# Kernel optimization log

Hardware: AMD Instinct MI355X
Metric: run time of the kernel (lower is better)

The kernel has to match this reference:

```python
import jax, jax.numpy as jnp
import numpy as np

EPS = 1e-5

def conv3x3(x, W, b):
    # NCHW 3x3 conv, padding=1 (SAME)
    y = jax.lax.conv_general_dilated(x, W, (1, 1), ((1, 1), (1, 1)),
                                     dimension_numbers=('NCHW', 'OIHW', 'NCHW'))
    return y + b[None, :, None, None]

def bn_relu(x, gamma, beta):
    # BatchNorm2d in training mode: batch statistics over (N,H,W)
    m = x.mean(axis=(0, 2, 3), keepdims=True)
    v = x.var(axis=(0, 2, 3), keepdims=True)
    xn = (x - m) * jax.lax.rsqrt(v + EPS)
    return jax.nn.relu(xn * gamma[None, :, None, None] + beta[None, :, None, None])

def haar_dwt2(x):
    # pywt.dwt2(x, 'db1') for even H,W: cA=LL, cH=row-detail/col-approx,
    # cV=row-approx/col-detail, cD=HH; each 0.5*(+-a +-b +-c +-d)
    a = x[:, :, 0::2, 0::2]
    b = x[:, :, 0::2, 1::2]
    c = x[:, :, 1::2, 0::2]
    d = x[:, :, 1::2, 1::2]
    cA = (a + b + c + d) * 0.5
    cH = (a + b - c - d) * 0.5
    cV = (a - b + c - d) * 0.5
    cD = (a - b - c + d) * 0.5
    return jnp.concatenate([cA, cH, cV, cD], axis=1)  # [B, 4C, H/2, W/2]

def setup_inputs() -> dict:
    key = jax.random.key(0)
    ks = jax.random.split(key, 4)
    B, Cin, Cout, H, W = 8, 64, 128, 256, 256
    inputs = jax.random.normal(ks[0], (B, Cin, H, W), dtype=jnp.float32)
    W1 = jax.random.normal(ks[1], (Cout, Cin, 3, 3), dtype=jnp.float32) * 0.05
    W2 = jax.random.normal(ks[2], (Cout, Cout, 3, 3), dtype=jnp.float32) * 0.05
    W3 = jax.random.normal(ks[3], (Cout, 4 * Cout, 3, 3), dtype=jnp.float32) * 0.05
    z = jnp.zeros((Cout,), jnp.float32)
    o = jnp.ones((Cout,), jnp.float32)
    return {"inputs": inputs,
            "W1": W1, "b1": z, "g1": o, "be1": z,
            "W2": W2, "b2": z, "g2": o, "be2": z,
            "W3": W3, "b3": z, "g3": o, "be3": z}

def reference(inputs, W1, b1, g1, be1, W2, b2, g2, be2, W3, b3, g3, be3):
    h = bn_relu(conv3x3(inputs, W1, b1), g1, be1)
    skip_con = bn_relu(conv3x3(h, W2, b2), g2, be2)          # [B, out_c, H, W]
    # original detaches before the pywt round-trip
    dwt = haar_dwt2(jax.lax.stop_gradient(skip_con))          # [B, 4*out_c, H/2, W/2]
    dwt_out = bn_relu(conv3x3(dwt, W3, b3), g3, be3)          # [B, out_c, H/2, W/2]
    return (skip_con, dwt_out)
```

## Files before the change

### kernel.cpp

```cpp
#include <hip/hip_runtime.h>

typedef __attribute__((ext_vector_type(8))) short bf16x8;
typedef __attribute__((ext_vector_type(4))) short bf16x4;
typedef __attribute__((ext_vector_type(4))) float f32x4;

__device__ __forceinline__ float bf2f(ushort u) {
  union { unsigned int i; float f; } v; v.i = ((unsigned int)u) << 16; return v.f;
}
__device__ __forceinline__ ushort f2bf(float f) {
  union { float f; unsigned int i; } v; v.f = f;
  unsigned int x = v.i;
  unsigned int r = (x + 0x7fffu + ((x >> 16) & 1u)) >> 16;
  return (ushort)r;
}

__global__ void zero_f32(float* p, int n) {
  int i = blockIdx.x * 256 + threadIdx.x;
  if (i < n) p[i] = 0.f;
}

__global__ void pack_w(const float* __restrict__ W, ushort* __restrict__ Wp, int Cin) {
  int ncic = Cin >> 5;
  int total = 9 * ncic * 8 * 64 * 8;
  for (int idx = blockIdx.x * 256 + threadIdx.x; idx < total; idx += gridDim.x * 256) {
    int j = idx & 7;
    int l = (idx >> 3) & 63;
    int cf = (idx >> 9) & 7;
    int rest = idx >> 12;
    int cic = rest % ncic;
    int tap = rest / ncic;
    int co = cf * 16 + (l & 15);
    int ci = cic * 32 + ((l >> 4) * 8) + j;
    int ky = tap / 3, kx = tap % 3;
    Wp[idx] = f2bf(W[((co * Cin + ci) * 3 + ky) * 3 + kx]);
  }
}

__global__ __launch_bounds__(256)
void nchw2nhwc(const float* __restrict__ in, ushort* __restrict__ out) {
  const int n  = blockIdx.y;
  const int p0 = blockIdx.x << 6;
  const int tid = threadIdx.x;
  __shared__ ushort t[64 * 72];
  {
    int c  = tid >> 2;
    int pq = (tid & 3) << 4;
    const float* ip = in + (((size_t)(n * 64 + c)) << 16) + p0 + pq;
#pragma unroll
    for (int k = 0; k < 4; ++k) {
      float4 f = *(const float4*)(ip + k * 4);
      int p = pq + k * 4;
      t[(p + 0) * 72 + c] = f2bf(f.x);
      t[(p + 1) * 72 + c] = f2bf(f.y);
      t[(p + 2) * 72 + c] = f2bf(f.z);
      t[(p + 3) * 72 + c] = f2bf(f.w);
    }
  }
  __syncthreads();
#pragma unroll
  for (int k = 0; k < 2; ++k) {
    int id = k * 256 + tid;
    int cj = id & 7, p = id >> 3;
    bf16x8 v = *(const bf16x8*)&t[p * 72 + cj * 8];
    *(bf16x8*)(out + ((((size_t)n << 16) + p0 + p) << 6) + cj * 8) = v;
  }
}

__device__ __forceinline__ bf16x8 bnrelu8(bf16x8 v, const float* __restrict__ coef, int c0) {
  float4 a0 = *(const float4*)(coef + c0);
  float4 a1 = *(const float4*)(coef + c0 + 4);
  float4 b0 = *(const float4*)(coef + 128 + c0);
  float4 b1 = *(const float4*)(coef + 128 + c0 + 4);
  bf16x8 r;
  r[0] = (short)f2bf(fmaxf(a0.x * bf2f((ushort)v[0]) + b0.x, 0.f));
  r[1] = (short)f2bf(fmaxf(a0.y * bf2f((ushort)v[1]) + b0.y, 0.f));
  r[2] = (short)f2bf(fmaxf(a0.z * bf2f((ushort)v[2]) + b0.z, 0.f));
  r[3] = (short)f2bf(fmaxf(a0.w * bf2f((ushort)v[3]) + b0.w, 0.f));
  r[4] = (short)f2bf(fmaxf(a1.x * bf2f((ushort)v[4]) + b1.x, 0.f));
  r[5] = (short)f2bf(fmaxf(a1.y * bf2f((ushort)v[5]) + b1.y, 0.f));
  r[6] = (short)f2bf(fmaxf(a1.z * bf2f((ushort)v[6]) + b1.z, 0.f));
  r[7] = (short)f2bf(fmaxf(a1.w * bf2f((ushort)v[7]) + b1.w, 0.f));
  return r;
}

template<int MODE>
__global__ __launch_bounds__(256)
void conv_mfma(const ushort* __restrict__ src, const ushort* __restrict__ Wp,
               const float* __restrict__ bias, const float* __restrict__ coef,
               ushort* __restrict__ out, float* __restrict__ sSum, float* __restrict__ sSsq,
               int Cin, int H, int W)
{
  const int ncic = Cin >> 5;
  const int x0 = blockIdx.x << 6;
  const int y0 = blockIdx.y << 1;
  const int n  = blockIdx.z;
  const int tid = threadIdx.x;
  const int wv = tid >> 6, l = tid & 63, l15 = l & 15, l4 = l >> 4;

  __shared__ __align__(16) char smem[17408];
  ushort* lds = (ushort*)smem;
  ushort* eps = (ushort*)smem;

  f32x4 acc[2][2][4];
#pragma unroll
  for (int yr = 0; yr < 2; ++yr)
#pragma unroll
    for (int f = 0; f < 2; ++f)
#pragma unroll
      for (int xf = 0; xf < 4; ++xf) acc[yr][f][xf] = (f32x4){0.f, 0.f, 0.f, 0.f};

  const size_t HW = (size_t)H * W;

  for (int cic = 0; cic < ncic; ++cic) {
    __syncthreads();
    for (int i = tid; i < 1056; i += 256) {
      int cj = i & 3;
      int t = i >> 2;
      int row = t / 66;
      int xt = t - row * 66;
      int ry = y0 + row - 1;
      int gx = x0 + xt - 1;
      bf16x8 v = {};
      if ((unsigned)ry < (unsigned)H && (unsigned)gx < (unsigned)W) {
        const ushort* p = src + ((size_t)n * HW + (size_t)ry * W + gx) * Cin + (cic << 5) + (cj << 3);
        v = *(const bf16x8*)p;
        if (MODE == 1) v = bnrelu8(v, coef, (cic << 5) + (cj << 3));
      }
      *(bf16x8*)&lds[(((row << 2) | cj) * 66 + xt) << 3] = v;
    }
    __syncthreads();

#pragma unroll
    for (int tap = 0; tap < 9; ++tap) {
      const int ky = tap / 3, kx = tap % 3;
      bf16x8 afr[2];
#pragma unroll
      for (int f = 0; f < 2; ++f) {
        const int cf = (wv << 1) | f;
        afr[f] = *(const bf16x8*)(Wp + (((size_t)(tap * ncic + cic) * 8 + cf) * 64 + l) * 8);
      }
      bf16x8 bfr[2][4];
#pragma unroll
      for (int yr = 0; yr < 2; ++yr)
#pragma unroll
        for (int xf = 0; xf < 4; ++xf) {
          int row = yr + ky;
          int xt = (xf << 4) + l15 + kx;
          bfr[yr][xf] = *(const bf16x8*)&lds[(((row << 2) | l4) * 66 + xt) << 3];
        }
#pragma unroll
      for (int f = 0; f < 2; ++f)
#pragma unroll
        for (int yr = 0; yr < 2; ++yr)
#pragma unroll
          for (int xf = 0; xf < 4; ++xf)
            acc[yr][f][xf] = __builtin_amdgcn_mfma_f32_16x16x32_bf16(afr[f], bfr[yr][xf], acc[yr][f][xf], 0, 0, 0);
    }
  }

  float sm[2][4] = {{0.f}}, sq[2][4] = {{0.f}};
  const int cb = (wv << 5) + (l4 << 2);
  for (int yr = 0; yr < 2; ++yr) {
    __syncthreads();
#pragma unroll
    for (int f = 0; f < 2; ++f) {
      const int cf = cb + (f << 4);
      float4 bv = *(const float4*)(bias + cf);
#pragma unroll
      for (int xf = 0; xf < 4; ++xf) {
        float v0 = acc[yr][f][xf][0] + bv.x;
        float v1 = acc[yr][f][xf][1] + bv.y;
        float v2 = acc[yr][f][xf][2] + bv.z;
        float v3 = acc[yr][f][xf][3] + bv.w;
        sm[f][0] += v0; sq[f][0] += v0 * v0;
        sm[f][1] += v1; sq[f][1] += v1 * v1;
        sm[f][2] += v2; sq[f][2] += v2 * v2;
        sm[f][3] += v3; sq[f][3] += v3 * v3;
        bf16x4 u;
        u[0] = (short)f2bf(v0); u[1] = (short)f2bf(v1);
        u[2] = (short)f2bf(v2); u[3] = (short)f2bf(v3);
        *(bf16x4*)&eps[((xf << 4) + l15) * 136 + cf] = u;
      }
    }
    __syncthreads();
    {
      const int xx = tid >> 2, c0 = (tid & 3) << 5;
      ushort* op = out + ((size_t)n * HW + (size_t)(y0 + yr) * W + x0 + xx) * 128 + c0;
#pragma unroll
      for (int k = 0; k < 4; ++k) {
        bf16x8 v = *(const bf16x8*)&eps[xx * 136 + c0 + (k << 3)];
        *(bf16x8*)(op + (k << 3)) = v;
      }
    }
  }

  const int rep = (int)((blockIdx.z * gridDim.y + blockIdx.y) * gridDim.x + blockIdx.x) & 31;
#pragma unroll
  for (int f = 0; f < 2; ++f)
#pragma unroll
    for (int j = 0; j < 4; ++j) {
      float s = sm[f][j], q = sq[f][j];
#pragma unroll
      for (int o = 1; o < 16; o <<= 1) { s += __shfl_xor(s, o); q += __shfl_xor(q, o); }
      if (l15 == 0) {
        int co = cb + (f << 4) + j;
        atomicAdd(&sSum[rep * 128 + co], s);
        atomicAdd(&sSsq[rep * 128 + co], q);
      }
    }
}

__global__ void bn_finalize(const float* __restrict__ sSum, const float* __restrict__ sSsq,
                            const float* __restrict__ g, const float* __restrict__ be,
                            float* __restrict__ coef, float invN)
{
  int c = threadIdx.x;
  float S = 0.f, Q = 0.f;
  for (int r = 0; r < 32; ++r) { S += sSum[r * 128 + c]; Q += sSsq[r * 128 + c]; }
  float m = S * invN;
  float v = Q * invN - m * m;
  float a = g[c] / sqrtf(v + 1e-5f);
  coef[c] = a;
  coef[128 + c] = be[c] - m * a;
}

__global__ __launch_bounds__(256)
void bn_transpose_out(const ushort* __restrict__ src, const float* __restrict__ coef,
                      float* __restrict__ dst, int H, int W)
{
  const int n  = blockIdx.z >> 2;
  const int cc = blockIdx.z & 3;
  const int x0 = blockIdx.x << 6;
  const int y  = blockIdx.y;
  const int tid = threadIdx.x;
  __shared__ float t[32 * 68];
  const size_t HW = (size_t)H * W;
  {
    int p = tid >> 2, cj = tid & 3;
    int c0 = (cc << 5) + (cj << 3);
    bf16x8 v = *(const bf16x8*)(src + ((size_t)n * HW + (size_t)y * W + x0 + p) * 128 + c0);
    float4 a0 = *(const float4*)(coef + c0);
    float4 a1 = *(const float4*)(coef + c0 + 4);
    float4 b0 = *(const float4*)(coef + 128 + c0);
    float4 b1 = *(const float4*)(coef + 128 + c0 + 4);
    int cl = cj << 3;
    t[(cl + 0) * 68 + p] = fmaxf(a0.x * bf2f((ushort)v[0]) + b0.x, 0.f);
    t[(cl + 1) * 68 + p] = fmaxf(a0.y * bf2f((ushort)v[1]) + b0.y, 0.f);
    t[(cl + 2) * 68 + p] = fmaxf(a0.z * bf2f((ushort)v[2]) + b0.z, 0.f);
    t[(cl + 3) * 68 + p] = fmaxf(a0.w * bf2f((ushort)v[3]) + b0.w, 0.f);
    t[(cl + 4) * 68 + p] = fmaxf(a1.x * bf2f((ushort)v[4]) + b1.x, 0.f);
    t[(cl + 5) * 68 + p] = fmaxf(a1.y * bf2f((ushort)v[5]) + b1.y, 0.f);
    t[(cl + 6) * 68 + p] = fmaxf(a1.z * bf2f((ushort)v[6]) + b1.z, 0.f);
    t[(cl + 7) * 68 + p] = fmaxf(a1.w * bf2f((ushort)v[7]) + b1.w, 0.f);
  }
  __syncthreads();
  {
    int c = tid >> 3, x8 = (tid & 7) << 3;
    float4 r0 = *(const float4*)&t[c * 68 + x8];
    float4 r1 = *(const float4*)&t[c * 68 + x8 + 4];
    float* op = dst + ((size_t)(n * 128 + (cc << 5) + c)) * HW + (size_t)y * W + x0 + x8;
    *(float4*)op = r0;
    *(float4*)(op + 4) = r1;
  }
}

__global__ __launch_bounds__(256)
void dwt_nhwc(const ushort* __restrict__ src, const float* __restrict__ coef,
              ushort* __restrict__ dwt)
{
  int idx = blockIdx.x * 256 + threadIdx.x;
  int cj = idx & 15;
  int ox = (idx >> 4) & 127;
  int oy = (idx >> 11) & 127;
  int n  = idx >> 18;
  int c0 = cj << 3;
  size_t base = (((size_t)n << 16) + (size_t)(oy * 2) * 256 + ox * 2) * 128 + c0;
  bf16x8 u00 = *(const bf16x8*)(src + base);
  bf16x8 u01 = *(const bf16x8*)(src + base + 128);
  bf16x8 u10 = *(const bf16x8*)(src + base + 256 * 128);
  bf16x8 u11 = *(const bf16x8*)(src + base + 256 * 128 + 128);
  float4 a0 = *(const float4*)(coef + c0);
  float4 a1 = *(const float4*)(coef + c0 + 4);
  float4 b0 = *(const float4*)(coef + 128 + c0);
  float4 b1 = *(const float4*)(coef + 128 + c0 + 4);
  float av[8] = {a0.x, a0.y, a0.z, a0.w, a1.x, a1.y, a1.z, a1.w};
  float bv[8] = {b0.x, b0.y, b0.z, b0.w, b1.x, b1.y, b1.z, b1.w};
  bf16x8 oA, oH, oV, oD;
#pragma unroll
  for (int k = 0; k < 8; ++k) {
    float p00 = fmaxf(av[k] * bf2f((ushort)u00[k]) + bv[k], 0.f);
    float p01 = fmaxf(av[k] * bf2f((ushort)u01[k]) + bv[k], 0.f);
    float p10 = fmaxf(av[k] * bf2f((ushort)u10[k]) + bv[k], 0.f);
    float p11 = fmaxf(av[k] * bf2f((ushort)u11[k]) + bv[k], 0.f);
    oA[k] = (short)f2bf((p00 + p01 + p10 + p11) * 0.5f);
    oH[k] = (short)f2bf((p00 + p01 - p10 - p11) * 0.5f);
    oV[k] = (short)f2bf((p00 - p01 + p10 - p11) * 0.5f);
    oD[k] = (short)f2bf((p00 - p01 - p10 + p11) * 0.5f);
  }
  size_t db = (((size_t)n << 14) + oy * 128 + ox) * 512 + c0;
  *(bf16x8*)(dwt + db)       = oA;
  *(bf16x8*)(dwt + db + 128) = oH;
  *(bf16x8*)(dwt + db + 256) = oV;
  *(bf16x8*)(dwt + db + 384) = oD;
}

extern "C" void kernel_launch(void* const* d_in, const int* in_sizes, int n_in,
                              void* d_out, int out_size, void* d_ws, size_t ws_size,
                              hipStream_t stream)
{
  const float* input = (const float*)d_in[0];
  const float* W1  = (const float*)d_in[1];
  const float* b1  = (const float*)d_in[2];
  const float* g1  = (const float*)d_in[3];
  const float* be1 = (const float*)d_in[4];
  const float* W2  = (const float*)d_in[5];
  const float* b2  = (const float*)d_in[6];
  const float* g2  = (const float*)d_in[7];
  const float* be2 = (const float*)d_in[8];
  const float* W3  = (const float*)d_in[9];
  const float* b3  = (const float*)d_in[10];
  const float* g3  = (const float*)d_in[11];
  const float* be3 = (const float*)d_in[12];

  char* ws = (char*)d_ws;
  ushort* h_raw    = (ushort*)(ws + 0);
  ushort* skip_raw = (ushort*)(ws + 134217728);
  ushort* dwt      = (ushort*)(ws + 268435456);
  ushort* in_nhwc  = (ushort*)(ws + 268435456);
  ushort* raw3     = (ushort*)(ws + 402653184);
  float*  stats    = (float*)(ws + 436207616);
  float*  s1 = stats,          *q1 = stats + 4096;
  float*  s2 = stats + 8192,   *q2 = stats + 12288;
  float*  s3 = stats + 16384,  *q3 = stats + 20480;
  float*  coef = (float*)(ws + 436305920);
  float*  c1 = coef, *c2 = coef + 256, *c3 = coef + 512;
  ushort* Wp1 = (ushort*)(ws + 436308992);
  ushort* Wp2 = (ushort*)(ws + 436456448);
  ushort* Wp3 = (ushort*)(ws + 436751360);

  zero_f32<<<96, 256, 0, stream>>>(stats, 24576);
  pack_w<<<288, 256, 0, stream>>>(W1, Wp1, 64);
  pack_w<<<576, 256, 0, stream>>>(W2, Wp2, 128);
  pack_w<<<2304, 256, 0, stream>>>(W3, Wp3, 512);
  nchw2nhwc<<<dim3(1024, 8), 256, 0, stream>>>(input, in_nhwc);

  conv_mfma<0><<<dim3(4, 128, 8), 256, 0, stream>>>(in_nhwc, Wp1, b1, nullptr,
                                                    h_raw, s1, q1, 64, 256, 256);
  bn_finalize<<<1, 128, 0, stream>>>(s1, q1, g1, be1, c1, 1.f / 524288.f);

  conv_mfma<1><<<dim3(4, 128, 8), 256, 0, stream>>>(h_raw, Wp2, b2, c1,
                                                    skip_raw, s2, q2, 128, 256, 256);
  bn_finalize<<<1, 128, 0, stream>>>(s2, q2, g2, be2, c2, 1.f / 524288.f);

  bn_transpose_out<<<dim3(4, 256, 32), 256, 0, stream>>>(skip_raw, c2, (float*)d_out, 256, 256);
  dwt_nhwc<<<8192, 256, 0, stream>>>(skip_raw, c2, dwt);

  conv_mfma<0><<<dim3(2, 64, 8), 256, 0, stream>>>(dwt, Wp3, b3, nullptr,
                                                   raw3, s3, q3, 512, 128, 128);
  bn_finalize<<<1, 128, 0, stream>>>(s3, q3, g3, be3, c3, 1.f / 131072.f);

  bn_transpose_out<<<dim3(2, 128, 32), 256, 0, stream>>>(raw3, c3, (float*)d_out + 67108864, 128, 128);
}
```

Before: 726.6 us.

## Double-buffer conv LDS tiles, prefetch fragments, and fuse skip output with DWT

The conv kernel now double-buffers its input tile in shared memory. The next channel chunk is loaded into registers while the current one is computed, which drops one barrier per chunk. Work is remapped so each wave owns one output row and four 16-channel fragments, and weight and LDS fragments for the next tap are prefetched. Separately, the skip BN/ReLU transpose output and the Haar DWT are fused into one kernel so skip_raw is read once instead of twice. The cost is more registers and twice the LDS per block, which may reduce occupancy.

```diff
diff --git a/kernel.cpp b/kernel.cpp
--- a/kernel.cpp
+++ b/kernel.cpp
@@ -96,90 +96,127 @@
   const int n  = blockIdx.z;
   const int tid = threadIdx.x;
   const int wv = tid >> 6, l = tid & 63, l15 = l & 15, l4 = l >> 4;
-
-  __shared__ __align__(16) char smem[17408];
-  ushort* lds = (ushort*)smem;
-  ushort* eps = (ushort*)smem;
-
-  f32x4 acc[2][2][4];
-#pragma unroll
-  for (int yr = 0; yr < 2; ++yr)
-#pragma unroll
-    for (int f = 0; f < 2; ++f)
-#pragma unroll
-      for (int xf = 0; xf < 4; ++xf) acc[yr][f][xf] = (f32x4){0.f, 0.f, 0.f, 0.f};
+  const int cg = wv >> 1;
+  const int wy = wv & 1;
+  const int cg4 = cg << 2;
+
+  __shared__ __align__(16) ushort smem[2 * 8448];
 
   const size_t HW = (size_t)H * W;
-
+  const ushort* srcn = src + (size_t)n * HW * Cin;
+
+  f32x4 acc[4][4];
+#pragma unroll
+  for (int f = 0; f < 4; ++f)
+#pragma unroll
+    for (int xf = 0; xf < 4; ++xf) acc[f][xf] = (f32x4){0.f, 0.f, 0.f, 0.f};
+
+  bf16x8 st[5];
+
+  auto LOADREG = [&](int cic) {
+#pragma unroll
+    for (int it = 0; it < 5; ++it) {
+      if (it < 4 || tid < 32) {
+        int i = it * 256 + tid;
+        int cj = i & 3, p = i >> 2;
+        int row = p / 66, xt = p - row * 66;
+        int ry = y0 + row - 1, gx = x0 + xt - 1;
+        bf16x8 v = {};
+        if ((unsigned)ry < (unsigned)H && (unsigned)gx < (unsigned)W)
+          v = *(const bf16x8*)(srcn + ((size_t)ry * W + gx) * Cin + (cic << 5) + (cj << 3));
+        st[it] = v;
+      }
+    }
+  };
+
+  auto WRITE = [&](ushort* buf, int cic) {
+#pragma unroll
+    for (int it = 0; it < 5; ++it) {
+      if (it < 4 || tid < 32) {
+        int i = it * 256 + tid;
+        bf16x8 v = st[it];
+        if (MODE == 1) {
+          int cj = i & 3, p = i >> 2;
+          int row = p / 66, xt = p - row * 66;
+          int ry = y0 + row - 1, gx = x0 + xt - 1;
+          if ((unsigned)ry < (unsigned)H && (unsigned)gx < (unsigned)W)
+            v = bnrelu8(v, coef, (cic << 5) + (cj << 3));
+        }
+        *(bf16x8*)(buf + i * 8) = v;
+      }
+    }
+  };
+
+  auto COMPUTE = [&](const ushort* buf, int cic) {
+    const ushort* lrow = buf + l15 * 32 + l4 * 8;
+    const ushort* wp = Wp + ((size_t)cic * 8 + cg4) * 512 + (size_t)l * 8;
+    const size_t tapstride = (size_t)ncic * 8 * 512;
+    bf16x8 aC[4], bC[4], aN[4], bN[4];
+#pragma unroll
+    for (int f = 0; f < 4; ++f) aC[f] = *(const bf16x8*)(wp + f * 512);
+#pragma unroll
+    for (int xf = 0; xf < 4; ++xf)
+      bC[xf] = *(const bf16x8*)(lrow + (wy * 66 + xf * 16) * 32);
+#pragma unroll
+    for (int tap = 0; tap < 9; ++tap) {
+      if (tap < 8) {
+        const int ky1 = (tap + 1) / 3, kx1 = (tap + 1) % 3;
+#pragma unroll
+        for (int f = 0; f < 4; ++f)
+          aN[f] = *(const bf16x8*)(wp + (size_t)(tap + 1) * tapstride + f * 512);
+#pragma unroll
+        for (int xf = 0; xf < 4; ++xf)
+          bN[xf] = *(const bf16x8*)(lrow + ((wy + ky1) * 66 + xf * 16 + kx1) * 32);
+      }
+#pragma unroll
+      for (int f = 0; f < 4; ++f)
+#pragma unroll
+        for (int xf = 0; xf < 4; ++xf)
+          acc[f][xf] = __builtin_amdgcn_mfma_f32_16x16x32_bf16(aC[f], bC[xf], acc[f][xf], 0, 0, 0);
+#pragma unroll
+      for (int f = 0; f < 4; ++f) aC[f] = aN[f];
+#pragma unroll
+      for (int xf = 0; xf < 4; ++xf) bC[xf] = bN[xf];
+    }
+  };
+
+  LOADREG(0);
+  WRITE(smem, 0);
+  __syncthreads();
+
+  int cur = 0;
   for (int cic = 0; cic < ncic; ++cic) {
+    if (cic + 1 < ncic) LOADREG(cic + 1);
+    COMPUTE(smem + cur * 8448, cic);
+    if (cic + 1 < ncic) WRITE(smem + (cur ^ 1) * 8448, cic + 1);
     __syncthreads();
-    for (int i = tid; i < 1056; i += 256) {
-      int cj = i & 3;
-      int t = i >> 2;
-      int row = t / 66;
-      int xt = t - row * 66;
-      int ry = y0 + row - 1;
-      int gx = x0 + xt - 1;
-      bf16x8 v = {};
-      if ((unsigned)ry < (unsigned)H && (unsigned)gx < (unsigned)W) {
-        const ushort* p = src + ((size_t)n * HW + (size_t)ry * W + gx) * Cin + (cic << 5) + (cj << 3);
-        v = *(const bf16x8*)p;
-        if (MODE == 1) v = bnrelu8(v, coef, (cic << 5) + (cj << 3));
-      }
-      *(bf16x8*)&lds[(((row << 2) | cj) * 66 + xt) << 3] = v;
-    }
-    __syncthreads();
-
-#pragma unroll
-    for (int tap = 0; tap < 9; ++tap) {
-      const int ky = tap / 3, kx = tap % 3;
-      bf16x8 afr[2];
-#pragma unroll
-      for (int f = 0; f < 2; ++f) {
-        const int cf = (wv << 1) | f;
-        afr[f] = *(const bf16x8*)(Wp + (((size_t)(tap * ncic + cic) * 8 + cf) * 64 + l) * 8);
-      }
-      bf16x8 bfr[2][4];
-#pragma unroll
-      for (int yr = 0; yr < 2; ++yr)
-#pragma unroll
-        for (int xf = 0; xf < 4; ++xf) {
-          int row = yr + ky;
-          int xt = (xf << 4) + l15 + kx;
-          bfr[yr][xf] = *(const bf16x8*)&lds[(((row << 2) | l4) * 66 + xt) << 3];
-        }
-#pragma unroll
-      for (int f = 0; f < 2; ++f)
-#pragma unroll
-        for (int yr = 0; yr < 2; ++yr)
-#pragma unroll
-          for (int xf = 0; xf < 4; ++xf)
-            acc[yr][f][xf] = __builtin_amdgcn_mfma_f32_16x16x32_bf16(afr[f], bfr[yr][xf], acc[yr][f][xf], 0, 0, 0);
-    }
-  }
-
-  float sm[2][4] = {{0.f}}, sq[2][4] = {{0.f}};
-  const int cb = (wv << 5) + (l4 << 2);
+    cur ^= 1;
+  }
+
+  float smv[4][4] = {{0.f}}, sqv[4][4] = {{0.f}};
+  ushort* eps = smem;
   for (int yr = 0; yr < 2; ++yr) {
     __syncthreads();
-#pragma unroll
-    for (int f = 0; f < 2; ++f) {
-      const int cf = cb + (f << 4);
-      float4 bv = *(const float4*)(bias + cf);
-#pragma unroll
-      for (int xf = 0; xf < 4; ++xf) {
-        float v0 = acc[yr][f][xf][0] + bv.x;
-        float v1 = acc[yr][f][xf][1] + bv.y;
-        float v2 = acc[yr][f][xf][2] + bv.z;
-        float v3 = acc[yr][f][xf][3] + bv.w;
-        sm[f][0] += v0; sq[f][0] += v0 * v0;
-        sm[f][1] += v1; sq[f][1] += v1 * v1;
-        sm[f][2] += v2; sq[f][2] += v2 * v2;
-        sm[f][3] += v3; sq[f][3] += v3 * v3;
-        bf16x4 u;
-        u[0] = (short)f2bf(v0); u[1] = (short)f2bf(v1);
-        u[2] = (short)f2bf(v2); u[3] = (short)f2bf(v3);
-        *(bf16x4*)&eps[((xf << 4) + l15) * 136 + cf] = u;
+    if (wy == yr) {
+#pragma unroll
+      for (int f = 0; f < 4; ++f) {
+        const int col = (cg << 6) + (f << 4) + (l4 << 2);
+        float4 bv = *(const float4*)(bias + col);
+#pragma unroll
+        for (int xf = 0; xf < 4; ++xf) {
+          float v0 = acc[f][xf][0] + bv.x;
+          float v1 = acc[f][xf][1] + bv.y;
+          float v2 = acc[f][xf][2] + bv.z;
+          float v3 = acc[f][xf][3] + bv.w;
+          smv[f][0] += v0; sqv[f][0] += v0 * v0;
+          smv[f][1] += v1; sqv[f][1] += v1 * v1;
+          smv[f][2] += v2; sqv[f][2] += v2 * v2;
+          smv[f][3] += v3; sqv[f][3] += v3 * v3;
+          bf16x4 u;
+          u[0] = (short)f2bf(v0); u[1] = (short)f2bf(v1);
+          u[2] = (short)f2bf(v2); u[3] = (short)f2bf(v3);
+          *(bf16x4*)&eps[((xf << 4) + l15) * 136 + col] = u;
+        }
       }
     }
     __syncthreads();
@@ -187,23 +224,21 @@
       const int xx = tid >> 2, c0 = (tid & 3) << 5;
       ushort* op = out + ((size_t)n * HW + (size_t)(y0 + yr) * W + x0 + xx) * 128 + c0;
 #pragma unroll
-      for (int k = 0; k < 4; ++k) {
-        bf16x8 v = *(const bf16x8*)&eps[xx * 136 + c0 + (k << 3)];
-        *(bf16x8*)(op + (k << 3)) = v;
-      }
+      for (int k = 0; k < 4; ++k)
+        *(bf16x8*)(op + (k << 3)) = *(const bf16x8*)&eps[xx * 136 + c0 + (k << 3)];
     }
   }
 
   const int rep = (int)((blockIdx.z * gridDim.y + blockIdx.y) * gridDim.x + blockIdx.x) & 31;
 #pragma unroll
-  for (int f = 0; f < 2; ++f)
+  for (int f = 0; f < 4; ++f)
 #pragma unroll
     for (int j = 0; j < 4; ++j) {
-      float s = sm[f][j], q = sq[f][j];
+      float s = smv[f][j], q = sqv[f][j];
 #pragma unroll
       for (int o = 1; o < 16; o <<= 1) { s += __shfl_xor(s, o); q += __shfl_xor(q, o); }
       if (l15 == 0) {
-        int co = cb + (f << 4) + j;
+        int co = (cg << 6) + (f << 4) + (l4 << 2) + j;
         atomicAdd(&sSum[rep * 128 + co], s);
         atomicAdd(&sSsq[rep * 128 + co], q);
       }
@@ -222,6 +257,73 @@
   float a = g[c] / sqrtf(v + 1e-5f);
   coef[c] = a;
   coef[128 + c] = be[c] - m * a;
+}
+
+__global__ __launch_bounds__(256)
+void skip_dwt2(const ushort* __restrict__ skipRaw, const float* __restrict__ coef,
+               float* __restrict__ outSkip, ushort* __restrict__ dwt)
+{
+  const int x0 = blockIdx.x << 6;
+  const int oy = blockIdx.y;
+  const int n  = blockIdx.z >> 2;
+  const int ct = blockIdx.z & 3;
+  const int y0 = oy << 1;
+  const int tid = threadIdx.x;
+  __shared__ float t32[32 * 2 * 68];
+
+#pragma unroll
+  for (int it = 0; it < 2; ++it) {
+    int i = it * 256 + tid;
+    int cj = i & 3, x = (i >> 2) & 63, r = i >> 8;
+    int c0 = (ct << 5) + (cj << 3);
+    bf16x8 v = *(const bf16x8*)(skipRaw + (((size_t)n << 16) + (size_t)(y0 + r) * 256 + x0 + x) * 128 + c0);
+    float4 a0 = *(const float4*)(coef + c0);
+    float4 a1 = *(const float4*)(coef + c0 + 4);
+    float4 b0 = *(const float4*)(coef + 128 + c0);
+    float4 b1 = *(const float4*)(coef + 128 + c0 + 4);
+    float av[8] = {a0.x, a0.y, a0.z, a0.w, a1.x, a1.y, a1.z, a1.w};
+    float bv[8] = {b0.x, b0.y, b0.z, b0.w, b1.x, b1.y, b1.z, b1.w};
+    int cl = cj << 3;
+#pragma unroll
+    for (int k = 0; k < 8; ++k)
+      t32[((cl + k) * 2 + r) * 68 + x] = fmaxf(av[k] * bf2f((ushort)v[k]) + bv[k], 0.f);
+  }
+  __syncthreads();
+
+  {
+    int c = tid >> 3, x8 = (tid & 7) << 3;
+    float* op = outSkip + (((size_t)(n * 128 + (ct << 5) + c)) << 16) + (size_t)y0 * 256 + x0 + x8;
+#pragma unroll
+    for (int r = 0; r < 2; ++r) {
+      float4 r0 = *(const float4*)&t32[(c * 2 + r) * 68 + x8];
+      float4 r1 = *(const float4*)&t32[(c * 2 + r) * 68 + x8 + 4];
+      *(float4*)(op + (size_t)r * 256) = r0;
+      *(float4*)(op + (size_t)r * 256 + 4) = r1;
+    }
+  }
+
+  if (tid < 128) {
+    int cj = tid & 3, ox = tid >> 2;
+    int cl = cj << 3;
+    bf16x8 oA, oH, oV, oD;
+#pragma unroll
+    for (int k = 0; k < 8; ++k) {
+      int c = cl + k;
+      float p00 = t32[(c * 2 + 0) * 68 + 2 * ox];
+      float p01 = t32[(c * 2 + 0) * 68 + 2 * ox + 1];
+      float p10 = t32[(c * 2 + 1) * 68 + 2 * ox];
+      float p11 = t32[(c * 2 + 1) * 68 + 2 * ox + 1];
+      oA[k] = (short)f2bf((p00 + p01 + p10 + p11) * 0.5f);
+      oH[k] = (short)f2bf((p00 + p01 - p10 - p11) * 0.5f);
+      oV[k] = (short)f2bf((p00 - p01 + p10 - p11) * 0.5f);
+      oD[k] = (short)f2bf((p00 - p01 - p10 + p11) * 0.5f);
+    }
+    size_t db = ((size_t)n * 16384 + (size_t)oy * 128 + (x0 >> 1) + ox) * 512 + (ct << 5) + cl;
+    *(bf16x8*)(dwt + db)       = oA;
+    *(bf16x8*)(dwt + db + 128) = oH;
+    *(bf16x8*)(dwt + db + 256) = oV;
+    *(bf16x8*)(dwt + db + 384) = oD;
+  }
 }
 
 __global__ __launch_bounds__(256)
@@ -264,46 +366,6 @@
   }
 }
 
-__global__ __launch_bounds__(256)
-void dwt_nhwc(const ushort* __restrict__ src, const float* __restrict__ coef,
-              ushort* __restrict__ dwt)
-{
-  int idx = blockIdx.x * 256 + threadIdx.x;
-  int cj = idx & 15;
-  int ox = (idx >> 4) & 127;
-  int oy = (idx >> 11) & 127;
-  int n  = idx >> 18;
-  int c0 = cj << 3;
-  size_t base = (((size_t)n << 16) + (size_t)(oy * 2) * 256 + ox * 2) * 128 + c0;
-  bf16x8 u00 = *(const bf16x8*)(src + base);
-  bf16x8 u01 = *(const bf16x8*)(src + base + 128);
-  bf16x8 u10 = *(const bf16x8*)(src + base + 256 * 128);
-  bf16x8 u11 = *(const bf16x8*)(src + base + 256 * 128 + 128);
-  float4 a0 = *(const float4*)(coef + c0);
-  float4 a1 = *(const float4*)(coef + c0 + 4);
-  float4 b0 = *(const float4*)(coef + 128 + c0);
-  float4 b1 = *(const float4*)(coef + 128 + c0 + 4);
-  float av[8] = {a0.x, a0.y, a0.z, a0.w, a1.x, a1.y, a1.z, a1.w};
-  float bv[8] = {b0.x, b0.y, b0.z, b0.w, b1.x, b1.y, b1.z, b1.w};
-  bf16x8 oA, oH, oV, oD;
-#pragma unroll
-  for (int k = 0; k < 8; ++k) {
-    float p00 = fmaxf(av[k] * bf2f((ushort)u00[k]) + bv[k], 0.f);
-    float p01 = fmaxf(av[k] * bf2f((ushort)u01[k]) + bv[k], 0.f);
-    float p10 = fmaxf(av[k] * bf2f((ushort)u10[k]) + bv[k], 0.f);
-    float p11 = fmaxf(av[k] * bf2f((ushort)u11[k]) + bv[k], 0.f);
-    oA[k] = (short)f2bf((p00 + p01 + p10 + p11) * 0.5f);
-    oH[k] = (short)f2bf((p00 + p01 - p10 - p11) * 0.5f);
-    oV[k] = (short)f2bf((p00 - p01 + p10 - p11) * 0.5f);
-    oD[k] = (short)f2bf((p00 - p01 - p10 + p11) * 0.5f);
-  }
-  size_t db = (((size_t)n << 14) + oy * 128 + ox) * 512 + c0;
-  *(bf16x8*)(dwt + db)       = oA;
-  *(bf16x8*)(dwt + db + 128) = oH;
-  *(bf16x8*)(dwt + db + 256) = oV;
-  *(bf16x8*)(dwt + db + 384) = oD;
-}
-
 extern "C" void kernel_launch(void* const* d_in, const int* in_sizes, int n_in,
                               void* d_out, int out_size, void* d_ws, size_t ws_size,
                               hipStream_t stream)
@@ -352,8 +414,7 @@
                                                     skip_raw, s2, q2, 128, 256, 256);
   bn_finalize<<<1, 128, 0, stream>>>(s2, q2, g2, be2, c2, 1.f / 524288.f);
 
-  bn_transpose_out<<<dim3(4, 256, 32), 256, 0, stream>>>(skip_raw, c2, (float*)d_out, 256, 256);
-  dwt_nhwc<<<8192, 256, 0, stream>>>(skip_raw, c2, dwt);
+  skip_dwt2<<<dim3(4, 128, 32), 256, 0, stream>>>(skip_raw, c2, (float*)d_out, dwt);
 
   conv_mfma<0><<<dim3(2, 64, 8), 256, 0, stream>>>(dwt, Wp3, b3, nullptr,
                                                    raw3, s3, q3, 512, 128, 128);
```

After: 992.9 us. 1.37x slower.

## Fuse skip BN-transpose output with Haar DWT and repack weights per-lane

Applied to the files above, without the earlier changes.

Merges the skip-connection BN+ReLU NCHW write and the Haar DWT into one kernel that reads each two-row tile of the raw conv output once, normalizes it into LDS, and emits both the fp32 skip output and the bf16 DWT coefficients. This removes a second full read of skip_raw and one kernel launch. Separately, the packed weight layout is reordered so each lane's nine taps and two fragments sit contiguously, giving a simpler base pointer and more local weight loads in the conv inner loop. The fused kernel uses more shared memory per block and only half the threads do the DWT stage.

```diff
diff --git a/kernel.cpp b/kernel.cpp
--- a/kernel.cpp
+++ b/kernel.cpp
@@ -21,16 +21,18 @@
 
 __global__ void pack_w(const float* __restrict__ W, ushort* __restrict__ Wp, int Cin) {
   int ncic = Cin >> 5;
-  int total = 9 * ncic * 8 * 64 * 8;
+  int total = ncic * 4 * 64 * 9 * 2 * 8;
   for (int idx = blockIdx.x * 256 + threadIdx.x; idx < total; idx += gridDim.x * 256) {
     int j = idx & 7;
-    int l = (idx >> 3) & 63;
-    int cf = (idx >> 9) & 7;
-    int rest = idx >> 12;
-    int cic = rest % ncic;
-    int tap = rest / ncic;
-    int co = cf * 16 + (l & 15);
-    int ci = cic * 32 + ((l >> 4) * 8) + j;
+    int f = (idx >> 3) & 1;
+    int rest = idx >> 4;
+    int tap = rest % 9;  rest /= 9;
+    int l = rest & 63;
+    int pc = rest >> 6;
+    int pair = pc & 3;
+    int cic = pc >> 2;
+    int co = ((pair << 1) | f) * 16 + (l & 15);
+    int ci = (cic << 5) + ((l >> 4) << 3) + j;
     int ky = tap / 3, kx = tap % 3;
     Wp[idx] = f2bf(W[((co * Cin + ci) * 3 + ky) * 3 + kx]);
   }
@@ -130,15 +132,15 @@
     }
     __syncthreads();
 
+    const ushort* wp = Wp + (((size_t)(cic * 4 + wv) * 64 + l) * 144);
+
 #pragma unroll
     for (int tap = 0; tap < 9; ++tap) {
       const int ky = tap / 3, kx = tap % 3;
       bf16x8 afr[2];
 #pragma unroll
-      for (int f = 0; f < 2; ++f) {
-        const int cf = (wv << 1) | f;
-        afr[f] = *(const bf16x8*)(Wp + (((size_t)(tap * ncic + cic) * 8 + cf) * 64 + l) * 8);
-      }
+      for (int f = 0; f < 2; ++f)
+        afr[f] = *(const bf16x8*)(wp + (tap * 2 + f) * 8);
       bf16x8 bfr[2][4];
 #pragma unroll
       for (int yr = 0; yr < 2; ++yr)
@@ -187,10 +189,8 @@
       const int xx = tid >> 2, c0 = (tid & 3) << 5;
       ushort* op = out + ((size_t)n * HW + (size_t)(y0 + yr) * W + x0 + xx) * 128 + c0;
 #pragma unroll
-      for (int k = 0; k < 4; ++k) {
-        bf16x8 v = *(const bf16x8*)&eps[xx * 136 + c0 + (k << 3)];
-        *(bf16x8*)(op + (k << 3)) = v;
-      }
+      for (int k = 0; k < 4; ++k)
+        *(bf16x8*)(op + (k << 3)) = *(const bf16x8*)&eps[xx * 136 + c0 + (k << 3)];
     }
   }
 
@@ -222,6 +222,73 @@
   float a = g[c] / sqrtf(v + 1e-5f);
   coef[c] = a;
   coef[128 + c] = be[c] - m * a;
+}
+
+__global__ __launch_bounds__(256)
+void skip_dwt2(const ushort* __restrict__ skipRaw, const float* __restrict__ coef,
+               float* __restrict__ outSkip, ushort* __restrict__ dwt)
+{
+  const int x0 = blockIdx.x << 6;
+  const int oy = blockIdx.y;
+  const int n  = blockIdx.z >> 2;
+  const int ct = blockIdx.z & 3;
+  const int y0 = oy << 1;
+  const int tid = threadIdx.x;
+  __shared__ float t32[32 * 2 * 68];
+
+#pragma unroll
+  for (int it = 0; it < 2; ++it) {
+    int i = it * 256 + tid;
+    int cj = i & 3, x = (i >> 2) & 63, r = i >> 8;
+    int c0 = (ct << 5) + (cj << 3);
+    bf16x8 v = *(const bf16x8*)(skipRaw + (((size_t)n << 16) + (size_t)(y0 + r) * 256 + x0 + x) * 128 + c0);
+    float4 a0 = *(const float4*)(coef + c0);
+    float4 a1 = *(const float4*)(coef + c0 + 4);
+    float4 b0 = *(const float4*)(coef + 128 + c0);
+    float4 b1 = *(const float4*)(coef + 128 + c0 + 4);
+    float av[8] = {a0.x, a0.y, a0.z, a0.w, a1.x, a1.y, a1.z, a1.w};
+    float bv[8] = {b0.x, b0.y, b0.z, b0.w, b1.x, b1.y, b1.z, b1.w};
+    int cl = cj << 3;
+#pragma unroll
+    for (int k = 0; k < 8; ++k)
+      t32[((cl + k) * 2 + r) * 68 + x] = fmaxf(av[k] * bf2f((ushort)v[k]) + bv[k], 0.f);
+  }
+  __syncthreads();
+
+  {
+    int c = tid >> 3, x8 = (tid & 7) << 3;
+    float* op = outSkip + (((size_t)(n * 128 + (ct << 5) + c)) << 16) + (size_t)y0 * 256 + x0 + x8;
+#pragma unroll
+    for (int r = 0; r < 2; ++r) {
+      float4 r0 = *(const float4*)&t32[(c * 2 + r) * 68 + x8];
+      float4 r1 = *(const float4*)&t32[(c * 2 + r) * 68 + x8 + 4];
+      *(float4*)(op + (size_t)r * 256) = r0;
+      *(float4*)(op + (size_t)r * 256 + 4) = r1;
+    }
+  }
+
+  if (tid < 128) {
+    int cj = tid & 3, ox = tid >> 2;
+    int cl = cj << 3;
+    bf16x8 oA, oH, oV, oD;
+#pragma unroll
+    for (int k = 0; k < 8; ++k) {
+      int c = cl + k;
+      float p00 = t32[(c * 2 + 0) * 68 + 2 * ox];
+      float p01 = t32[(c * 2 + 0) * 68 + 2 * ox + 1];
+      float p10 = t32[(c * 2 + 1) * 68 + 2 * ox];
+      float p11 = t32[(c * 2 + 1) * 68 + 2 * ox + 1];
+      oA[k] = (short)f2bf((p00 + p01 + p10 + p11) * 0.5f);
+      oH[k] = (short)f2bf((p00 + p01 - p10 - p11) * 0.5f);
+      oV[k] = (short)f2bf((p00 - p01 + p10 - p11) * 0.5f);
+      oD[k] = (short)f2bf((p00 - p01 - p10 + p11) * 0.5f);
+    }
+    size_t db = ((size_t)n * 16384 + (size_t)oy * 128 + (x0 >> 1) + ox) * 512 + (ct << 5) + cl;
+    *(bf16x8*)(dwt + db)       = oA;
+    *(bf16x8*)(dwt + db + 128) = oH;
+    *(bf16x8*)(dwt + db + 256) = oV;
+    *(bf16x8*)(dwt + db + 384) = oD;
+  }
 }
 
 __global__ __launch_bounds__(256)
@@ -264,46 +331,6 @@
   }
 }
 
-__global__ __launch_bounds__(256)
-void dwt_nhwc(const ushort* __restrict__ src, const float* __restrict__ coef,
-              ushort* __restrict__ dwt)
-{
-  int idx = blockIdx.x * 256 + threadIdx.x;
-  int cj = idx & 15;
-  int ox = (idx >> 4) & 127;
-  int oy = (idx >> 11) & 127;
-  int n  = idx >> 18;
-  int c0 = cj << 3;
-  size_t base = (((size_t)n << 16) + (size_t)(oy * 2) * 256 + ox * 2) * 128 + c0;
-  bf16x8 u00 = *(const bf16x8*)(src + base);
-  bf16x8 u01 = *(const bf16x8*)(src + base + 128);
-  bf16x8 u10 = *(const bf16x8*)(src + base + 256 * 128);
-  bf16x8 u11 = *(const bf16x8*)(src + base + 256 * 128 + 128);
-  float4 a0 = *(const float4*)(coef + c0);
-  float4 a1 = *(const float4*)(coef + c0 + 4);
-  float4 b0 = *(const float4*)(coef + 128 + c0);
-  float4 b1 = *(const float4*)(coef + 128 + c0 + 4);
-  float av[8] = {a0.x, a0.y, a0.z, a0.w, a1.x, a1.y, a1.z, a1.w};
-  float bv[8] = {b0.x, b0.y, b0.z, b0.w, b1.x, b1.y, b1.z, b1.w};
-  bf16x8 oA, oH, oV, oD;
-#pragma unroll
-  for (int k = 0; k < 8; ++k) {
-    float p00 = fmaxf(av[k] * bf2f((ushort)u00[k]) + bv[k], 0.f);
-    float p01 = fmaxf(av[k] * bf2f((ushort)u01[k]) + bv[k], 0.f);
-    float p10 = fmaxf(av[k] * bf2f((ushort)u10[k]) + bv[k], 0.f);
-    float p11 = fmaxf(av[k] * bf2f((ushort)u11[k]) + bv[k], 0.f);
-    oA[k] = (short)f2bf((p00 + p01 + p10 + p11) * 0.5f);
-    oH[k] = (short)f2bf((p00 + p01 - p10 - p11) * 0.5f);
-    oV[k] = (short)f2bf((p00 - p01 + p10 - p11) * 0.5f);
-    oD[k] = (short)f2bf((p00 - p01 - p10 + p11) * 0.5f);
-  }
-  size_t db = (((size_t)n << 14) + oy * 128 + ox) * 512 + c0;
-  *(bf16x8*)(dwt + db)       = oA;
-  *(bf16x8*)(dwt + db + 128) = oH;
-  *(bf16x8*)(dwt + db + 256) = oV;
-  *(bf16x8*)(dwt + db + 384) = oD;
-}
-
 extern "C" void kernel_launch(void* const* d_in, const int* in_sizes, int n_in,
                               void* d_out, int out_size, void* d_ws, size_t ws_size,
                               hipStream_t stream)
@@ -352,8 +379,7 @@
                                                     skip_raw, s2, q2, 128, 256, 256);
   bn_finalize<<<1, 128, 0, stream>>>(s2, q2, g2, be2, c2, 1.f / 524288.f);
 
-  bn_transpose_out<<<dim3(4, 256, 32), 256, 0, stream>>>(skip_raw, c2, (float*)d_out, 256, 256);
-  dwt_nhwc<<<8192, 256, 0, stream>>>(skip_raw, c2, dwt);
+  skip_dwt2<<<dim3(4, 128, 32), 256, 0, stream>>>(skip_raw, c2, (float*)d_out, dwt);
 
   conv_mfma<0><<<dim3(2, 64, 8), 256, 0, stream>>>(dwt, Wp3, b3, nullptr,
                                                    raw3, s3, q3, 512, 128, 128);
```

Result: slower. 847.8 us (+16.7%).
